# Performance work log

Hardware: AMD Instinct MI355X
Metric: run time of the kernel (lower is better)

The kernel has to match this reference:

```python
import jax, jax.numpy as jnp
import numpy as np

NEG_SLOPE = 0.2


def setup_inputs() -> dict:
    key = jax.random.key(0)
    ks = jax.random.split(key, 12)
    Nm, Na, E, Din, H, D = 50000, 50000, 400000, 128, 8, 32
    return {
        "master_feats": jax.random.normal(ks[0], (Nm, Din), jnp.float32),
        "attn_feats0": jax.random.normal(ks[1], (Na, Din), jnp.float32),
        "attn_feats1": jax.random.normal(ks[2], (Na, Din), jnp.float32),
        "src0": jax.random.randint(ks[3], (E,), 0, Na, jnp.int32),
        "dst0": jax.random.randint(ks[4], (E,), 0, Nm, jnp.int32),
        "src1": jax.random.randint(ks[5], (E,), 0, Na, jnp.int32),
        "dst1": jax.random.randint(ks[6], (E,), 0, Nm, jnp.int32),
        "W_master": jax.random.normal(ks[7], (Din, H * D), jnp.float32) * 0.08,
        "W0": jax.random.normal(ks[8], (Din, H * D), jnp.float32) * 0.08,
        "W1": jax.random.normal(ks[9], (Din, H * D), jnp.float32) * 0.08,
        "attn_l": jax.random.normal(ks[10], (H, D), jnp.float32) * 0.1,
        "attn_r": jax.random.normal(ks[11], (H, D), jnp.float32) * 0.1,
    }


def reference(master_feats, attn_feats0, attn_feats1, src0, dst0, src1, dst1,
              W_master, W0, W1, attn_l, attn_r):
    Nm = master_feats.shape[0]
    H, D = attn_l.shape

    # Per-node-type linear projections (no bias) + attention logits.
    ft_m = (master_feats @ W_master).reshape(Nm, H, D)        # [Nm,H,D]
    er = jnp.einsum("nhd,hd->nh", ft_m, attn_r)               # [Nm,H]

    def proj(feats, W):
        ft = (feats @ W).reshape(feats.shape[0], H, D)
        el = jnp.einsum("nhd,hd->nh", ft, attn_l)
        return ft, el

    ft0, el0 = proj(attn_feats0, W0)
    ft1, el1 = proj(attn_feats1, W1)

    lrelu = lambda x: jnp.where(x >= 0, x, NEG_SLOPE * x)
    e0 = lrelu(el0[src0] + er[dst0])                          # [E0,H]
    e1 = lrelu(el1[src1] + er[dst1])                          # [E1,H]

    # Heterograph edge softmax: normalize over ALL incoming edges of each
    # master node, regardless of source node type (subtract dst-max for
    # stability; mathematically identical to the conditional path in source).
    dst = jnp.concatenate([dst0, dst1])
    e = jnp.concatenate([e0, e1], axis=0)                     # [E0+E1,H]
    emax = jax.ops.segment_max(e, dst, num_segments=Nm)
    emax = jnp.where(jnp.isfinite(emax), emax, 0.0)           # nodes w/o edges
    ee = jnp.exp(e - emax[dst])
    esum = jax.ops.segment_sum(ee, dst, num_segments=Nm)
    a = ee / esum[dst]                                        # [E0+E1,H]

    # u_mul_e + sum aggregation onto master nodes.
    E0 = src0.shape[0]
    msg = jnp.concatenate(
        [ft0[src0] * a[:E0, :, None], ft1[src1] * a[E0:, :, None]], axis=0
    )                                                         # [E,H,D]
    rst = jax.ops.segment_sum(msg, dst, num_segments=Nm)      # [Nm,H,D]
    return rst
```

## Files before the change

kernel.cpp:

```cpp
#include <hip/hip_runtime.h>
#include <cstdint>
#include <cstddef>

#define NEG_SLOPE 0.2f

typedef __attribute__((ext_vector_type(8))) short short8;
typedef __attribute__((ext_vector_type(4))) float f32x4;

static __device__ __forceinline__ unsigned short f2bf(float x) {
  uint32_t u = __float_as_uint(x);
  uint32_t r = (u + 0x7FFFu + ((u >> 16) & 1u)) >> 16;
  return (unsigned short)r;
}

__global__ void prep_kernel(const float* __restrict__ W0, const float* __restrict__ W1,
                            const float* __restrict__ Wm, const float* __restrict__ ar,
                            unsigned short* __restrict__ T0, unsigned short* __restrict__ T1,
                            float* __restrict__ Q) {
  const int z = blockIdx.y;
  const int t = threadIdx.x;
  if (z < 2) {
    const float* W = (z == 0) ? W0 : W1;
    unsigned short* T = (z == 0) ? T0 : T1;
    int c = blockIdx.x * 2 + (t >> 7);
    int k = t & 127;
    T[c * 128 + k] = f2bf(W[k * 256 + c]);
  } else if (blockIdx.x == 0) {
    #pragma unroll
    for (int q4 = 0; q4 < 4; ++q4) {
      int t2 = q4 * 256 + t;
      int k = t2 >> 3, h = t2 & 7;
      const float* wr = &Wm[k * 256 + h * 32];
      const float* av = &ar[h * 32];
      float s = 0.f;
      #pragma unroll
      for (int q = 0; q < 8; ++q) {
        float4 w4 = *(const float4*)(wr + q * 4);
        float4 a4 = *(const float4*)(av + q * 4);
        s += w4.x * a4.x + w4.y * a4.y + w4.z * a4.z + w4.w * a4.w;
      }
      Q[h * 128 + k] = s;
    }
  }
}

__global__ __launch_bounds__(256)
void er_count_kernel(const float* __restrict__ feats, const float* __restrict__ Q,
                     float* __restrict__ er, int N, int erb,
                     const int* __restrict__ dst0, int E0,
                     const int* __restrict__ dst1, int E1,
                     int* __restrict__ deg) {
  const int t = threadIdx.x;
  if (blockIdx.x >= erb) {
    int i = (blockIdx.x - erb) * 256 + t;
    int E = E0 + E1;
    if (i < E) {
      int d = (i < E0) ? dst0[i] : dst1[i - E0];
      atomicAdd(&deg[d], 1);
    }
    return;
  }

  __shared__ float Qs[8 * 128];
  ((float4*)Qs)[t] = ((const float4*)Q)[t];
  __syncthreads();

  const int lane = t & 63, wave = t >> 6;
  const int j = lane & 7;
  const int n = blockIdx.x * 32 + wave * 8 + (lane >> 3);
  const bool ok = n < N;

  float acc[8] = {};
  #pragma unroll
  for (int q = 0; q < 4; ++q) {
    float4 f = make_float4(0.f, 0.f, 0.f, 0.f);
    int kc = q * 32 + j * 4;
    if (ok) f = *(const float4*)(&feats[(size_t)n * 128 + kc]);
    #pragma unroll
    for (int h = 0; h < 8; ++h) {
      const float* qr = &Qs[h * 128 + kc];
      acc[h] = fmaf(f.x, qr[0], acc[h]);
      acc[h] = fmaf(f.y, qr[1], acc[h]);
      acc[h] = fmaf(f.z, qr[2], acc[h]);
      acc[h] = fmaf(f.w, qr[3], acc[h]);
    }
  }
  #pragma unroll
  for (int h = 0; h < 8; ++h) {
    acc[h] += __shfl_xor(acc[h], 1);
    acc[h] += __shfl_xor(acc[h], 2);
    acc[h] += __shfl_xor(acc[h], 4);
  }
  float out = acc[0];
  out = (j == 1) ? acc[1] : out;  out = (j == 2) ? acc[2] : out;
  out = (j == 3) ? acc[3] : out;  out = (j == 4) ? acc[4] : out;
  out = (j == 5) ? acc[5] : out;  out = (j == 6) ? acc[6] : out;
  out = (j == 7) ? acc[7] : out;
  if (ok) er[(size_t)n * 8 + j] = out;
}

__global__ __launch_bounds__(256)
void proj_mfma_kernel(const float* __restrict__ fa0, const float* __restrict__ fa1,
                      const unsigned short* __restrict__ Wt0,
                      const unsigned short* __restrict__ Wt1,
                      const float* __restrict__ attn_l,
                      int Na0, int Na1,
                      unsigned short* __restrict__ ft_all, float* __restrict__ el_all) {
  const int z = blockIdx.z;
  const float* feats = (z == 0) ? fa0 : fa1;
  const unsigned short* Wt = (z == 0) ? Wt0 : Wt1;
  const float* av = attn_l;
  const int N = (z == 0) ? Na0 : Na1;
  unsigned short* ft_out = (z == 0) ? ft_all : ft_all + (size_t)Na0 * 256;
  float* el_out = (z == 0) ? el_all : el_all + (size_t)Na0 * 8;

  const int rb = blockIdx.x * 64;
  if (rb >= N) return;

  __shared__ unsigned short As[64 * 128];
  const int t = threadIdx.x;
  const int wid = t >> 6, lane = t & 63;
  const int l15 = lane & 15, l4 = lane >> 4;
  const int cbw = wid * 64;
  const int head0 = cbw >> 5;

  short8 bf[4][4];
  #pragma unroll
  for (int nf = 0; nf < 4; ++nf) {
    const unsigned short* wp = &Wt[(size_t)(cbw + nf * 16 + l15) * 128];
    #pragma unroll
    for (int kb = 0; kb < 4; ++kb)
      bf[kb][nf] = *(const short8*)(wp + kb * 32 + l4 * 8);
  }

  #pragma unroll
  for (int it = 0; it < 8; ++it) {
    int i = it * 256 + t;
    int r = i >> 5, kc = (i & 31) << 2;
    float4 f = make_float4(0.f, 0.f, 0.f, 0.f);
    if (rb + r < N) f = *(const float4*)(&feats[(size_t)(rb + r) * 128 + kc]);
    ushort4 u;
    u.x = f2bf(f.x); u.y = f2bf(f.y); u.z = f2bf(f.z); u.w = f2bf(f.w);
    uint32_t byte = ((uint32_t)(r * 256 + kc * 2)) ^ ((uint32_t)((r & 7) << 4));
    *(ushort4*)((char*)As + byte) = u;
  }
  __syncthreads();

  f32x4 acc[4][4];
  #pragma unroll
  for (int a = 0; a < 4; ++a)
    #pragma unroll
    for (int b = 0; b < 4; ++b)
      acc[a][b] = (f32x4){0.f, 0.f, 0.f, 0.f};

  #pragma unroll
  for (int kb = 0; kb < 4; ++kb) {
    short8 af[4];
    #pragma unroll
    for (int mf = 0; mf < 4; ++mf) {
      int row = mf * 16 + l15;
      uint32_t byte = ((uint32_t)(row * 256 + kb * 64 + l4 * 16)) ^ ((uint32_t)((row & 7) << 4));
      af[mf] = *(const short8*)((const char*)As + byte);
    }
    #pragma unroll
    for (int mf = 0; mf < 4; ++mf)
      #pragma unroll
      for (int nf = 0; nf < 4; ++nf)
        acc[mf][nf] = __builtin_amdgcn_mfma_f32_16x16x32_bf16(
            bf[kb][nf], af[mf], acc[mf][nf], 0, 0, 0);
  }

  float avf[4][4];
  #pragma unroll
  for (int nf = 0; nf < 4; ++nf)
    #pragma unroll
    for (int reg = 0; reg < 4; ++reg)
      avf[nf][reg] = av[(head0 + (nf >> 1)) * 32 + (nf & 1) * 16 + l4 * 4 + reg];

  #pragma unroll
  for (int mf = 0; mf < 4; ++mf) {
    int node = rb + mf * 16 + l15;
    bool ok = node < N;
    if (ok) {
      size_t base = (size_t)node * 256 + cbw + l4 * 4;
      #pragma unroll
      for (int nf = 0; nf < 4; ++nf) {
        ushort4 u;
        u.x = f2bf(acc[mf][nf][0]); u.y = f2bf(acc[mf][nf][1]);
        u.z = f2bf(acc[mf][nf][2]); u.w = f2bf(acc[mf][nf][3]);
        *(ushort4*)(&ft_out[base + nf * 16]) = u;
      }
    }
    #pragma unroll
    for (int hh = 0; hh < 2; ++hh) {
      float p = 0.f;
      #pragma unroll
      for (int reg = 0; reg < 4; ++reg) {
        p = fmaf(acc[mf][2 * hh][reg], avf[2 * hh][reg], p);
        p = fmaf(acc[mf][2 * hh + 1][reg], avf[2 * hh + 1][reg], p);
      }
      p += __shfl_xor(p, 16);
      p += __shfl_xor(p, 32);
      if (ok && l4 == 0)
        el_out[(size_t)node * 8 + head0 + hh] = p;
    }
  }
}

__global__ __launch_bounds__(1024)
void block_reduce_kernel(const int* __restrict__ deg, int* __restrict__ partial, int n) {
  __shared__ int wsum[16];
  const int t = threadIdx.x;
  int idx = blockIdx.x * 1024 + t;
  int v = (idx < n) ? deg[idx] : 0;
  #pragma unroll
  for (int off = 1; off < 64; off <<= 1) v += __shfl_xor(v, off);
  if ((t & 63) == 0) wsum[t >> 6] = v;
  __syncthreads();
  if (t < 16) {
    int x = wsum[t];
    #pragma unroll
    for (int off = 1; off < 16; off <<= 1) x += __shfl_xor(x, off);
    if (t == 0) partial[blockIdx.x] = x;
  }
}

__global__ __launch_bounds__(64)
void partial_scan_kernel(const int* __restrict__ partial, int* __restrict__ base,
                         int nb, int* __restrict__ offs, int n) {
  const int t = threadIdx.x;
  int v = (t < nb) ? partial[t] : 0;
  int incl = v;
  #pragma unroll
  for (int off = 1; off < 64; off <<= 1) {
    int x = __shfl_up(incl, off);
    if (t >= off) incl += x;
  }
  if (t < nb) base[t] = incl - v;
  if (t == nb - 1) offs[n] = incl;
}

__global__ __launch_bounds__(1024)
void apply_scan_kernel(const int* __restrict__ deg, const int* __restrict__ base,
                       int* __restrict__ offs, int* __restrict__ cursor, int n) {
  __shared__ int wsum[16];
  const int t = threadIdx.x;
  const int idx = blockIdx.x * 1024 + t;
  int v = (idx < n) ? deg[idx] : 0;
  const int lane = t & 63, w = t >> 6;
  int incl = v;
  #pragma unroll
  for (int off = 1; off < 64; off <<= 1) {
    int x = __shfl_up(incl, off);
    if (lane >= off) incl += x;
  }
  if (lane == 63) wsum[w] = incl;
  __syncthreads();
  if (t < 16) {
    int x = wsum[t];
    #pragma unroll
    for (int off = 1; off < 16; off <<= 1) {
      int y = __shfl_up(x, off);
      if (t >= off) x += y;
    }
    wsum[t] = x;
  }
  __syncthreads();
  int excl = base[blockIdx.x] + ((w > 0) ? wsum[w - 1] : 0) + incl - v;
  if (idx < n) {
    offs[idx] = excl;
    cursor[idx] = excl;
  }
}

__global__ void scatter_kernel(const int* __restrict__ src0, const int* __restrict__ dst0, int E0,
                               const int* __restrict__ src1, const int* __restrict__ dst1, int E1,
                               int* __restrict__ cursor, char* __restrict__ recs,
                               const float* __restrict__ el, const float* __restrict__ er,
                               int Na0) {
  int E = E0 + E1;
  int i = blockIdx.x * blockDim.x + threadIdx.x;
  if (i >= E) return;
  int s, d;
  if (i < E0) { s = src0[i]; d = dst0[i]; }
  else        { s = src1[i - E0] + Na0; d = dst1[i - E0]; }
  int pos = atomicAdd(&cursor[d], 1);

  const float* elp = &el[(size_t)s * 8];
  const float* erp = &er[(size_t)d * 8];
  float4 ea = *(const float4*)elp, eb = *(const float4*)(elp + 4);
  float4 ra = *(const float4*)erp, rb = *(const float4*)(erp + 4);
  float w[8];
  w[0] = ea.x + ra.x; w[1] = ea.y + ra.y; w[2] = ea.z + ra.z; w[3] = ea.w + ra.w;
  w[4] = eb.x + rb.x; w[5] = eb.y + rb.y; w[6] = eb.z + rb.z; w[7] = eb.w + rb.w;
  uint32_t pk[4];
  #pragma unroll
  for (int q = 0; q < 4; ++q) {
    float v0 = w[2 * q], v1 = w[2 * q + 1];
    v0 = fmaxf(v0, NEG_SLOPE * v0);
    v1 = fmaxf(v1, NEG_SLOPE * v1);
    uint32_t b0 = f2bf(__expf(v0)), b1 = f2bf(__expf(v1));
    pk[q] = b0 | (b1 << 16);
  }
  char* rp = recs + ((size_t)(uint32_t)pos << 5);
  *(uint4*)rp = make_uint4((uint32_t)s, pk[0], pk[1], pk[2]);
  *(uint32_t*)(rp + 16) = pk[3];
}

__global__ __launch_bounds__(256)
void aggregate_kernel(const int* __restrict__ offs, const char* __restrict__ recs,
                      const unsigned short* __restrict__ ft,
                      float* __restrict__ rst, int Nm) {
  int gid = blockIdx.x * blockDim.x + threadIdx.x;
  int n = gid >> 6;
  int lane = threadIdx.x & 63;
  if (n >= Nm) return;
  const int nu = __builtin_amdgcn_readfirstlane(n);
  const int beg = offs[nu], end = offs[nu + 1];
  const int h = lane >> 3;
  const char* ftl = (const char*)ft + lane * 8;
  float o0 = 0.f, o1 = 0.f, o2 = 0.f, o3 = 0.f;
  float sw = 0.f;

  #pragma unroll 8
  for (int i = beg; i < end; ++i) {
    const uint32_t* rp = (const uint32_t*)(recs + ((size_t)(uint32_t)i << 5));
    uint32_t sct = rp[0];
    uint32_t d0 = rp[1], d1 = rp[2], d2 = rp[3], d3 = rp[4];
    uint2 g = *(const uint2*)(ftl + ((size_t)sct << 9));
    uint32_t wa = (h & 2) ? d1 : d0;
    uint32_t wb = (h & 2) ? d3 : d2;
    uint32_t wsl = (h & 4) ? wb : wa;
    float w = __uint_as_float((h & 1) ? (wsl & 0xffff0000u) : (wsl << 16));
    sw += w;
    o0 = fmaf(w, __uint_as_float(g.x << 16), o0);
    o1 = fmaf(w, __uint_as_float(g.x & 0xffff0000u), o1);
    o2 = fmaf(w, __uint_as_float(g.y << 16), o2);
    o3 = fmaf(w, __uint_as_float(g.y & 0xffff0000u), o3);
  }

  if (beg < end) {
    float inv = 1.0f / sw;
    o0 *= inv; o1 *= inv; o2 *= inv; o3 *= inv;
  }
  *(float4*)(&rst[(size_t)n * 256 + lane * 4]) = make_float4(o0, o1, o2, o3);
}

extern "C" void kernel_launch(void* const* d_in, const int* in_sizes, int n_in,
                              void* d_out, int out_size, void* d_ws, size_t ws_size,
                              hipStream_t stream) {
  const float* master = (const float*)d_in[0];
  const float* af0    = (const float*)d_in[1];
  const float* af1    = (const float*)d_in[2];
  const int*   src0   = (const int*)d_in[3];
  const int*   dst0   = (const int*)d_in[4];
  const int*   src1   = (const int*)d_in[5];
  const int*   dst1   = (const int*)d_in[6];
  const float* Wm     = (const float*)d_in[7];
  const float* W0     = (const float*)d_in[8];
  const float* W1     = (const float*)d_in[9];
  const float* attn_l = (const float*)d_in[10];
  const float* attn_r = (const float*)d_in[11];

  const int Nm  = in_sizes[0] / 128;
  const int Na0 = in_sizes[1] / 128;
  const int Na1 = in_sizes[2] / 128;
  const int E0  = in_sizes[3];
  const int E1  = in_sizes[5];
  float* rst = (float*)d_out;

  char* ws = (char*)d_ws;
  size_t off = 0;
  auto alloc = [&](size_t b) -> char* {
    char* p = ws + off;
    off += (b + 511) & ~(size_t)511;
    return p;
  };
  unsigned short* ft = (unsigned short*)alloc((size_t)(Na0 + Na1) * 256 * sizeof(unsigned short));
  float* el = (float*)alloc((size_t)(Na0 + Na1) * 8 * sizeof(float));
  float* er = (float*)alloc((size_t)Nm * 8 * sizeof(float));
  unsigned short* Wt0 = (unsigned short*)alloc(256 * 128 * sizeof(unsigned short));
  unsigned short* Wt1 = (unsigned short*)alloc(256 * 128 * sizeof(unsigned short));
  float* Q     = (float*)alloc(8 * 128 * sizeof(float));
  int* deg     = (int*)alloc((size_t)Nm * sizeof(int));
  int* offs    = (int*)alloc((size_t)(Nm + 1) * sizeof(int));
  int* cursor  = (int*)alloc((size_t)Nm * sizeof(int));
  int* partial = (int*)alloc(64 * sizeof(int));
  int* pbase   = (int*)alloc(64 * sizeof(int));
  char* recs   = alloc((size_t)(E0 + E1) * 32);

  const int E = E0 + E1;
  hipMemsetAsync(deg, 0, (size_t)Nm * sizeof(int), stream);

  prep_kernel<<<dim3(128, 3), 256, 0, stream>>>(W0, W1, Wm, attn_r, Wt0, Wt1, Q);

  const int erb = (Nm + 31) / 32;
  const int cb  = (E + 255) / 256;
  er_count_kernel<<<erb + cb, 256, 0, stream>>>(master, Q, er, Nm, erb,
                                                dst0, E0, dst1, E1, deg);

  int Nmax = Na0 > Na1 ? Na0 : Na1;
  const int mb = (Nmax + 63) / 64;
  proj_mfma_kernel<<<dim3(mb, 1, 2), 256, 0, stream>>>(
      af0, af1, Wt0, Wt1, attn_l, Na0, Na1, ft, el);

  const int nb = (Nm + 1023) / 1024;
  block_reduce_kernel<<<nb, 1024, 0, stream>>>(deg, partial, Nm);
  partial_scan_kernel<<<1, 64, 0, stream>>>(partial, pbase, nb, offs, Nm);
  apply_scan_kernel<<<nb, 1024, 0, stream>>>(deg, pbase, offs, cursor, Nm);

  scatter_kernel<<<cb, 256, 0, stream>>>(src0, dst0, E0, src1, dst1, E1,
                                         cursor, recs, el, er, Na0);

  aggregate_kernel<<<(Nm + 3) / 4, 256, 0, stream>>>(offs, recs, ft, rst, Nm);
}
```

Baseline: 211.4 us.

## Fuse three-pass degree scan into single-pass decoupled lookback scan and fold memset

Replaces the reduce / partial-scan / apply-scan trio with one scan kernel that uses decoupled lookback over per-block state flags. The degree-array zeroing moves from a memset into an extra grid row of the prep kernel, which also clears the lookback state. This removes three launches and one extra pass over the degree array, in exchange for a serial spin-wait between blocks. That wait relies on earlier blocks being scheduled, which holds for 49 blocks.

```diff
diff --git a/kernel.cpp b/kernel.cpp
--- a/kernel.cpp
+++ b/kernel.cpp
@@ -16,7 +16,8 @@
 __global__ void prep_kernel(const float* __restrict__ W0, const float* __restrict__ W1,
                             const float* __restrict__ Wm, const float* __restrict__ ar,
                             unsigned short* __restrict__ T0, unsigned short* __restrict__ T1,
-                            float* __restrict__ Q) {
+                            float* __restrict__ Q, int* __restrict__ deg, int Nm,
+                            unsigned int* __restrict__ bstate) {
   const int z = blockIdx.y;
   const int t = threadIdx.x;
   if (z < 2) {
@@ -25,22 +26,29 @@
     int c = blockIdx.x * 2 + (t >> 7);
     int k = t & 127;
     T[c * 128 + k] = f2bf(W[k * 256 + c]);
-  } else if (blockIdx.x == 0) {
-    #pragma unroll
-    for (int q4 = 0; q4 < 4; ++q4) {
-      int t2 = q4 * 256 + t;
-      int k = t2 >> 3, h = t2 & 7;
-      const float* wr = &Wm[k * 256 + h * 32];
-      const float* av = &ar[h * 32];
-      float s = 0.f;
+  } else if (z == 2) {
+    if (blockIdx.x == 0) {
       #pragma unroll
-      for (int q = 0; q < 8; ++q) {
-        float4 w4 = *(const float4*)(wr + q * 4);
-        float4 a4 = *(const float4*)(av + q * 4);
-        s += w4.x * a4.x + w4.y * a4.y + w4.z * a4.z + w4.w * a4.w;
+      for (int q4 = 0; q4 < 4; ++q4) {
+        int t2 = q4 * 256 + t;
+        int k = t2 >> 3, h = t2 & 7;
+        const float* wr = &Wm[k * 256 + h * 32];
+        const float* av = &ar[h * 32];
+        float s = 0.f;
+        #pragma unroll
+        for (int q = 0; q < 8; ++q) {
+          float4 w4 = *(const float4*)(wr + q * 4);
+          float4 a4 = *(const float4*)(av + q * 4);
+          s += w4.x * a4.x + w4.y * a4.y + w4.z * a4.z + w4.w * a4.w;
+        }
+        Q[h * 128 + k] = s;
       }
-      Q[h * 128 + k] = s;
-    }
+    } else if (blockIdx.x == 1) {
+      if (t < 64) bstate[t] = 0u;
+    }
+  } else {
+    for (int i = blockIdx.x * 256 + t; i < Nm; i += 128 * 256)
+      deg[i] = 0;
   }
 }
 
@@ -208,44 +216,13 @@
 }
 
 __global__ __launch_bounds__(1024)
-void block_reduce_kernel(const int* __restrict__ deg, int* __restrict__ partial, int n) {
+void scan_kernel(const int* __restrict__ deg, int* __restrict__ offs,
+                 int* __restrict__ cursor, int n, int nb,
+                 unsigned int* __restrict__ bstate) {
+  const int b = blockIdx.x, t = threadIdx.x;
   __shared__ int wsum[16];
-  const int t = threadIdx.x;
-  int idx = blockIdx.x * 1024 + t;
-  int v = (idx < n) ? deg[idx] : 0;
-  #pragma unroll
-  for (int off = 1; off < 64; off <<= 1) v += __shfl_xor(v, off);
-  if ((t & 63) == 0) wsum[t >> 6] = v;
-  __syncthreads();
-  if (t < 16) {
-    int x = wsum[t];
-    #pragma unroll
-    for (int off = 1; off < 16; off <<= 1) x += __shfl_xor(x, off);
-    if (t == 0) partial[blockIdx.x] = x;
-  }
-}
-
-__global__ __launch_bounds__(64)
-void partial_scan_kernel(const int* __restrict__ partial, int* __restrict__ base,
-                         int nb, int* __restrict__ offs, int n) {
-  const int t = threadIdx.x;
-  int v = (t < nb) ? partial[t] : 0;
-  int incl = v;
-  #pragma unroll
-  for (int off = 1; off < 64; off <<= 1) {
-    int x = __shfl_up(incl, off);
-    if (t >= off) incl += x;
-  }
-  if (t < nb) base[t] = incl - v;
-  if (t == nb - 1) offs[n] = incl;
-}
-
-__global__ __launch_bounds__(1024)
-void apply_scan_kernel(const int* __restrict__ deg, const int* __restrict__ base,
-                       int* __restrict__ offs, int* __restrict__ cursor, int n) {
-  __shared__ int wsum[16];
-  const int t = threadIdx.x;
-  const int idx = blockIdx.x * 1024 + t;
+  __shared__ int s_base;
+  int idx = b * 1024 + t;
   int v = (idx < n) ? deg[idx] : 0;
   const int lane = t & 63, w = t >> 6;
   int incl = v;
@@ -266,7 +243,33 @@
     wsum[t] = x;
   }
   __syncthreads();
-  int excl = base[blockIdx.x] + ((w > 0) ? wsum[w - 1] : 0) + incl - v;
+  const int blockAgg = wsum[15];
+
+  if (t == 0) {
+    unsigned int pub = ((unsigned int)blockAgg << 2) | (b == 0 ? 2u : 1u);
+    __hip_atomic_store(&bstate[b], pub, __ATOMIC_RELEASE, __HIP_MEMORY_SCOPE_AGENT);
+    int exc = 0;
+    if (b > 0) {
+      int pb = b - 1;
+      while (true) {
+        unsigned int s = __hip_atomic_load(&bstate[pb], __ATOMIC_ACQUIRE,
+                                           __HIP_MEMORY_SCOPE_AGENT);
+        unsigned int st = s & 3u;
+        if (st == 0u) continue;
+        exc += (int)(s >> 2);
+        if (st == 2u) break;
+        --pb;
+      }
+      unsigned int pub2 = ((unsigned int)(exc + blockAgg) << 2) | 2u;
+      __hip_atomic_store(&bstate[b], pub2, __ATOMIC_RELEASE, __HIP_MEMORY_SCOPE_AGENT);
+    }
+    s_base = exc;
+    if (b == nb - 1) offs[n] = exc + blockAgg;
+  }
+  __syncthreads();
+
+  const int base = s_base;
+  int excl = base + ((w > 0) ? wsum[w - 1] : 0) + incl - v;
   if (idx < n) {
     offs[idx] = excl;
     cursor[idx] = excl;
@@ -385,14 +388,13 @@
   int* deg     = (int*)alloc((size_t)Nm * sizeof(int));
   int* offs    = (int*)alloc((size_t)(Nm + 1) * sizeof(int));
   int* cursor  = (int*)alloc((size_t)Nm * sizeof(int));
-  int* partial = (int*)alloc(64 * sizeof(int));
-  int* pbase   = (int*)alloc(64 * sizeof(int));
+  unsigned int* bstate = (unsigned int*)alloc(64 * sizeof(unsigned int));
   char* recs   = alloc((size_t)(E0 + E1) * 32);
 
   const int E = E0 + E1;
-  hipMemsetAsync(deg, 0, (size_t)Nm * sizeof(int), stream);
-
-  prep_kernel<<<dim3(128, 3), 256, 0, stream>>>(W0, W1, Wm, attn_r, Wt0, Wt1, Q);
+
+  prep_kernel<<<dim3(128, 4), 256, 0, stream>>>(W0, W1, Wm, attn_r,
+                                                Wt0, Wt1, Q, deg, Nm, bstate);
 
   const int erb = (Nm + 31) / 32;
   const int cb  = (E + 255) / 256;
@@ -405,9 +407,7 @@
       af0, af1, Wt0, Wt1, attn_l, Na0, Na1, ft, el);
 
   const int nb = (Nm + 1023) / 1024;
-  block_reduce_kernel<<<nb, 1024, 0, stream>>>(deg, partial, Nm);
-  partial_scan_kernel<<<1, 64, 0, stream>>>(partial, pbase, nb, offs, Nm);
-  apply_scan_kernel<<<nb, 1024, 0, stream>>>(deg, pbase, offs, cursor, Nm);
+  scan_kernel<<<nb, 1024, 0, stream>>>(deg, offs, cursor, Nm, nb, bstate);
 
   scatter_kernel<<<cb, 256, 0, stream>>>(src0, dst0, E0, src1, dst1, E1,
                                          cursor, recs, el, er, Na0);
```

New measurement: 210.6 us. Within noise of the previous version (-0.4%).
